# Kernel optimization log

Hardware: AMD Instinct MI355X
Metric: run time of the kernel (lower is better)

The kernel has to match this reference:

```python
import jax, jax.numpy as jnp
import numpy as np

MARGIN = 0.3
EPS = 0.1              # label smoothing weight
NUM_CLASSES = 100000
WEIGHT_T = 1.0
WEIGHT_X = 1.0
BATCH = 1024
EMBED_DIM = 512


def setup_inputs() -> dict:
    key = jax.random.key(0)
    k1, k2, k3 = jax.random.split(key, 3)
    x = jax.random.normal(k1, (BATCH, EMBED_DIM), dtype=jnp.float32)
    # classifier: weight ~ N(0, 0.01), bias = 0 (matches nn.init in module)
    W = jax.random.normal(k2, (NUM_CLASSES, EMBED_DIM), dtype=jnp.float32) * 0.01
    b = jnp.zeros((NUM_CLASSES,), dtype=jnp.float32)
    labels = jax.random.randint(k3, (BATCH,), 0, NUM_CLASSES)
    return {"x": x, "W": W, "b": b, "labels": labels}


def reference(x, W, b, labels):
    # ---- TripletLoss with batch-hard mining ----
    sq = jnp.sum(x * x, axis=1)                      # [B]
    dist = sq[:, None] + sq[None, :] - 2.0 * (x @ x.T)  # [B, B]
    dist = jnp.sqrt(jnp.clip(dist, 1e-12))
    same = labels[:, None] == labels[None, :]        # [B, B] (diagonal True)
    dist_ap = jnp.max(jnp.where(same, dist, -jnp.inf), axis=1)  # hardest positive
    dist_an = jnp.min(jnp.where(same, jnp.inf, dist), axis=1)   # hardest negative
    # MarginRankingLoss(dist_an, dist_ap, y=1) = mean(relu(dist_ap - dist_an + margin))
    triplet_loss = jnp.mean(jnp.maximum(dist_ap - dist_an + MARGIN, 0.0))

    # ---- CrossEntropy with label smoothing ----
    logits = x @ W.T + b                              # [B, K]
    log_probs = jax.nn.log_softmax(logits, axis=1)
    onehot = jax.nn.one_hot(labels, NUM_CLASSES, dtype=log_probs.dtype)
    targets = (1.0 - EPS) * onehot + EPS / NUM_CLASSES
    ce_loss = jnp.sum(jnp.mean(-targets * log_probs, axis=0))

    return WEIGHT_T * triplet_loss + WEIGHT_X * ce_loss
```

## Files before the change

### kernel.cpp

```cpp
#include <hip/hip_runtime.h>
#include <hip/hip_bf16.h>
#include <math.h>

#define B 1024
#define D 512
#define KC 100000
#define MARGIN 0.3f
#define EPSSM 0.1f
#define NCP 782
#define NCP_PAD 784

typedef __attribute__((ext_vector_type(8))) short bf16x8;
typedef __attribute__((ext_vector_type(4))) float f32x4;

__device__ __forceinline__ unsigned cvtpk(float lo, float hi) {
    union { __hip_bfloat162 h2; unsigned u; } cv;
    cv.h2 = __float22bfloat162_rn(make_float2(lo, hi));
    return cv.u;
}

__device__ __forceinline__ void async16(const void* g, void* l) {
    __builtin_amdgcn_global_load_lds((const __attribute__((address_space(1))) unsigned int*)g,
                                     (__attribute__((address_space(3))) unsigned int*)l,
                                     16, 0, 0);
}

#define VMCNT(n) asm volatile("s_waitcnt vmcnt(" #n ")" ::: "memory")
#define FENCE    asm volatile("" ::: "memory")


__global__ void init_ws(float* ws) {
    int i = blockIdx.x * blockDim.x + threadIdx.x;
    if (i < 2 * B) ws[i] = 0.f;
    else if (i < 3 * B) ((int*)ws)[i] = 0;
    else if (i < 4 * B) ((int*)ws)[i] = 0x7F800000;
}

__global__ __launch_bounds__(256) void prep_kernel(const float* __restrict__ x,
                                                   const float* __restrict__ W,
                                                   const float* __restrict__ bias,
                                                   const int* __restrict__ labels,
                                                   float* __restrict__ ws,
                                                   unsigned short* __restrict__ xp) {
    const int bid = blockIdx.x;
    const int tid = threadIdx.x;
    __shared__ float xs[8][D];
    __shared__ int labs[8];
    __shared__ float sqi[8];
    __shared__ float red_ap[8][4], red_an[8][4];

    if (bid >= 512) {
        int gid = (bid - 512) * 256 + tid;
        int region = gid >> 9;
        int u = gid & 511;
        int rloc = u >> 2, qpos = u & 3;
        int ku = qpos ^ ((rloc >> 1) & 3);
        int mb = region >> 4, kt = region & 15;
        const float* src = x + (size_t)(mb * 128 + rloc) * D + kt * 32 + ku * 8;
        f32x4 a = *(const f32x4*)src;
        f32x4 b2 = *(const f32x4*)(src + 4);
        unsigned pv[4] = { cvtpk(a[0], a[1]), cvtpk(a[2], a[3]), cvtpk(b2[0], b2[1]), cvtpk(b2[2], b2[3]) };
        *(uint4*)(xp + (size_t)region * 4096 + (size_t)u * 8) = *(uint4*)pv;
        return;
    }
    if (bid >= 256) {
        int wid = tid >> 6, lane = tid & 63;
        int row = (bid - 256) * 4 + wid;
        int lab = labels[row];
        const float* xr = x + (size_t)row * D;
        const float* wr = W + (size_t)lab * D;
        float dsum = 0.f;
#pragma unroll
        for (int u = 0; u < 2; ++u) {
            int k = (lane * 2 + u) * 4;
            float4 a = *(const float4*)&xr[k];
            float4 w = *(const float4*)&wr[k];
            dsum += a.x * w.x + a.y * w.y + a.z * w.z + a.w * w.w;
        }
        for (int o = 32; o >= 1; o >>= 1) dsum += __shfl_xor(dsum, o);
        if (lane == 0) atomicAdd(&ws[B + row], (1.f - EPSSM) * (dsum + bias[lab]));
        return;
    }

    const int row0 = (bid >> 1) * 8;
    const int jbase = (bid & 1) * 512;
    for (int f = tid; f < 8 * (D / 4); f += 256) {
        int r = f / (D / 4);
        int p = f % (D / 4);
        *(float4*)&xs[r][p * 4] = *(const float4*)&x[(size_t)(row0 + r) * D + p * 4];
    }
    if (tid < 8) labs[tid] = labels[row0 + tid];
    __syncthreads();
    if (tid < 8) {
        float s = 0.f;
        for (int k = 0; k < D; ++k) s += xs[tid][k] * xs[tid][k];
        sqi[tid] = s;
    }
    __syncthreads();

    float ap[8], an[8];
#pragma unroll
    for (int r = 0; r < 8; ++r) { ap[r] = -INFINITY; an[r] = INFINITY; }

    for (int j = jbase + tid; j < jbase + 512; j += 256) {
        int labj = labels[j];
        float dot[8];
        float sqj = 0.f;
#pragma unroll
        for (int r = 0; r < 8; ++r) dot[r] = 0.f;
        for (int kc = 0; kc < D; kc += 32) {
            float4 xj[8];
#pragma unroll
            for (int u = 0; u < 8; ++u) xj[u] = *(const float4*)&x[(size_t)j * D + kc + u * 4];
#pragma unroll
            for (int u = 0; u < 8; ++u)
                sqj += xj[u].x * xj[u].x + xj[u].y * xj[u].y + xj[u].z * xj[u].z + xj[u].w * xj[u].w;
#pragma unroll
            for (int r = 0; r < 8; ++r) {
                float d = 0.f;
#pragma unroll
                for (int u = 0; u < 8; ++u) {
                    const float4 a = *(const float4*)&xs[r][kc + u * 4];
                    d += a.x * xj[u].x + a.y * xj[u].y + a.z * xj[u].z + a.w * xj[u].w;
                }
                dot[r] += d;
            }
        }
#pragma unroll
        for (int r = 0; r < 8; ++r) {
            float d2 = sqi[r] + sqj - 2.f * dot[r];
            float dist = sqrtf(fmaxf(d2, 1e-12f));
            if (labj == labs[r]) ap[r] = fmaxf(ap[r], dist);
            else an[r] = fminf(an[r], dist);
        }
    }
#pragma unroll
    for (int r = 0; r < 8; ++r) {
        for (int o = 32; o >= 1; o >>= 1) {
            ap[r] = fmaxf(ap[r], __shfl_xor(ap[r], o));
            an[r] = fminf(an[r], __shfl_xor(an[r], o));
        }
    }
    int wid = tid >> 6;
    if ((tid & 63) == 0) {
#pragma unroll
        for (int r = 0; r < 8; ++r) { red_ap[r][wid] = ap[r]; red_an[r][wid] = an[r]; }
    }
    __syncthreads();
    if (tid < 8) {
        float a = -INFINITY, n = INFINITY;
#pragma unroll
        for (int w = 0; w < 4; ++w) { a = fmaxf(a, red_ap[tid][w]); n = fminf(n, red_an[tid][w]); }
        a = fmaxf(a, 0.f);
        int* apbits = (int*)(ws + 2 * B);
        int* anbits = (int*)(ws + 3 * B);
        atomicMax(&apbits[row0 + tid], __float_as_int(a));
        atomicMin(&anbits[row0 + tid], __float_as_int(n));
    }
}

__global__ __launch_bounds__(256, 3) void ce_gemm_d(const unsigned short* __restrict__ xp,
                                                    const float* __restrict__ W,
                                                    const float* __restrict__ bias,
                                                    float* __restrict__ ws) {
    const int b = blockIdx.x;
    const int xcd = b & 7, slot = b >> 3;
    const int cp = (slot >> 3) * 8 + xcd;
    const int mb = slot & 7;
    if (cp >= NCP) return;
    const int rowbase = mb * 128;
    const int cbase = cp * 128;

    __shared__ unsigned short lds[24576];

    const int tid = threadIdx.x;
    const int lane = tid & 63;
    const int wid = tid >> 6;
    const int wm = wid >> 1, wn = wid & 1;
    const int q = lane >> 4, l15 = lane & 15;

    f32x4 acc[4][4];
#pragma unroll
    for (int m = 0; m < 4; ++m)
#pragma unroll
        for (int n = 0; n < 4; ++n) acc[m][n] = (f32x4){0.f, 0.f, 0.f, 0.f};

#define STAGE(kt_) {                                                               \
        unsigned short* lA = &lds[((kt_) & 1) * 12288];                            \
        float* lB = (float*)&lds[((kt_) & 1) * 12288 + 4096];                      \
        const unsigned short* ga = xp + (size_t)(mb * 16 + (kt_)) * 4096;          \
        async16(ga + tid * 8, lA + tid * 8);                                       \
        async16(ga + 2048 + tid * 8, lA + 2048 + tid * 8);                         \
        _Pragma("unroll")                                                          \
        for (int i = 0; i < 4; ++i) {                                              \
            int u = i * 256 + tid;                                                 \
            int row = u >> 3;                                                      \
            int lu = (u & 7) ^ (row & 7);                                          \
            int rc = cbase + row; rc = rc < KC ? rc : KC - 1;                      \
            async16(&W[(size_t)rc * D + (kt_) * 32 + lu * 4], lB + u * 4);         \
        } }
#define READS(par_) {                                                              \
        const unsigned short* sA = &lds[(par_) * 12288];                           \
        const float* sB = (const float*)&lds[(par_) * 12288 + 4096];               \
        _Pragma("unroll") for (int m = 0; m < 4; ++m) {                            \
            int rl = wm * 64 + m * 16 + l15;                                       \
            af[m] = *(const bf16x8*)&sA[(rl * 4 + (q ^ ((rl >> 1) & 3))) * 8]; }   \
        _Pragma("unroll") for (int n = 0; n < 4; ++n) {                            \
            int rl = wn * 64 + n * 16 + l15;                                       \
            f32x4 b0 = *(const f32x4*)&sB[rl * 32 + ((q * 2) ^ (rl & 7)) * 4];     \
            f32x4 b1 = *(const f32x4*)&sB[rl * 32 + ((q * 2 + 1) ^ (rl & 7)) * 4]; \
            union { unsigned u[4]; bf16x8 v; } cv;                                 \
            cv.u[0] = cvtpk(b0[0], b0[1]); cv.u[1] = cvtpk(b0[2], b0[3]);          \
            cv.u[2] = cvtpk(b1[0], b1[1]); cv.u[3] = cvtpk(b1[2], b1[3]);          \
            bfr[n] = cv.v; } }
#define MFMAC() {                                                                  \
        __builtin_amdgcn_s_setprio(1);                                             \
        _Pragma("unroll") for (int m = 0; m < 4; ++m)                              \
        _Pragma("unroll") for (int n = 0; n < 4; ++n)                              \
            acc[m][n] = __builtin_amdgcn_mfma_f32_16x16x32_bf16(                   \
                af[m], bfr[n], acc[m][n], 0, 0, 0);                                \
        __builtin_amdgcn_s_setprio(0); }

    STAGE(0); STAGE(1);

    bf16x8 af[4], bfr[4];
#pragma unroll
    for (int kt = 0; kt < 16; ++kt) {
        const int par = kt & 1;
        if (kt < 15) { VMCNT(6); } else { VMCNT(0); }
        __builtin_amdgcn_s_barrier(); FENCE;
        READS(par);
        MFMAC();
        __builtin_amdgcn_s_barrier(); FENCE;
        if (kt + 2 < 16) STAGE(kt + 2);
    }
#undef STAGE
#undef READS
#undef MFMAC

    __syncthreads();
    float* redE = (float*)lds;
    float* redL = redE + 256;
    float biasv[4];
#pragma unroll
    for (int n = 0; n < 4; ++n) {
        int cc = cbase + wn * 64 + n * 16 + l15;
        biasv[n] = bias[cc < KC ? cc : KC - 1];
    }
#pragma unroll
    for (int m = 0; m < 4; ++m) {
#pragma unroll
        for (int r2 = 0; r2 < 4; ++r2) {
            float pe = 0.f, pl = 0.f;
#pragma unroll
            for (int n = 0; n < 4; ++n) {
                int cc = cbase + wn * 64 + n * 16 + l15;
                if (cc < KC) {
                    float lg = acc[m][n][r2] + biasv[n];
                    pe += __expf(lg);
                    pl += lg;
                }
            }
#pragma unroll
            for (int o = 1; o < 16; o <<= 1) {
                pe += __shfl_xor(pe, o);
                pl += __shfl_xor(pl, o);
            }
            if (l15 == 0) {
                int rowl = wm * 64 + m * 16 + q * 4 + r2;
                redE[rowl * 2 + wn] = pe;
                redL[rowl * 2 + wn] = pl;
            }
        }
    }
    __syncthreads();
    if (tid < 128) {
        float se = redE[tid * 2] + redE[tid * 2 + 1];
        float sl = redL[tid * 2] + redL[tid * 2 + 1];
        atomicAdd(&ws[rowbase + tid], se);
        atomicAdd(&ws[B + rowbase + tid], (EPSSM / (float)KC) * sl);
    }
}

__global__ __launch_bounds__(1024) void final_kernel(const float* __restrict__ ws,
                                                     float* __restrict__ out) {
    const float* sumexp = ws;
    const float* lin = ws + B;
    const int* apbits = (const int*)(ws + 2 * B);
    const int* anbits = (const int*)(ws + 3 * B);
    int i = threadIdx.x;
    float ce = logf(sumexp[i]) - lin[i];
    float ap = __int_as_float(apbits[i]);
    float an = __int_as_float(anbits[i]);
    float v = ce + fmaxf(ap - an + MARGIN, 0.f);
    for (int o = 32; o >= 1; o >>= 1) v += __shfl_xor(v, o);
    __shared__ float red[16];
    int wid = threadIdx.x >> 6, lane = threadIdx.x & 63;
    if (lane == 0) red[wid] = v;
    __syncthreads();
    if (threadIdx.x == 0) {
        float s = 0.f;
#pragma unroll
        for (int w = 0; w < 16; ++w) s += red[w];
        out[0] = s / (float)B;
    }
}

extern "C" void kernel_launch(void* const* d_in, const int* in_sizes, int n_in,
                              void* d_out, int out_size, void* d_ws, size_t ws_size,
                              hipStream_t stream) {
    const float* x = (const float*)d_in[0];
    const float* W = (const float*)d_in[1];
    const float* bias = (const float*)d_in[2];
    const int* labels = (const int*)d_in[3];
    float* out = (float*)d_out;
    float* ws = (float*)d_ws;

    unsigned short* xp = (unsigned short*)((char*)d_ws + 16384);

    init_ws<<<16, 256, 0, stream>>>(ws);
    prep_kernel<<<768, 256, 0, stream>>>(x, W, bias, labels, ws, xp);
    ce_gemm_d<<<8 * NCP_PAD, 256, 0, stream>>>(xp, W, bias, ws);
    final_kernel<<<1, 1024, 0, stream>>>(ws, out);
}
```

Measured before the change: 265.4 us.

## Enlarge CE GEMM tile to 256 rows, convert W to bf16 once in LDS

Raises the CE GEMM block tile from 128 to 256 batch rows, so each W tile is read from global memory half as many times, and launches half as many blocks. W is now loaded into registers three k-steps ahead, converted to bf16 by one thread, and written once into a double-buffered LDS slot. Previously every wave re-read fp32 W from LDS and converted it itself. The packed activations use a triple-buffered LDS ring with a matching 256-row packing layout in the prep kernel. The cost is 32 accumulator tiles per thread and more register pressure, with occupancy dropped to 2 blocks per SIMD group.

```diff
diff --git a/kernel.cpp b/kernel.cpp
--- a/kernel.cpp
+++ b/kernel.cpp
@@ -26,6 +26,7 @@
 }
 
 #define VMCNT(n) asm volatile("s_waitcnt vmcnt(" #n ")" ::: "memory")
+#define LGKM0    asm volatile("s_waitcnt lgkmcnt(0)" ::: "memory")
 #define FENCE    asm volatile("" ::: "memory")
 
 
@@ -51,16 +52,16 @@
 
     if (bid >= 512) {
         int gid = (bid - 512) * 256 + tid;
-        int region = gid >> 9;
-        int u = gid & 511;
-        int rloc = u >> 2, qpos = u & 3;
+        int region = gid >> 10;
+        int p = gid & 1023;
+        int rloc = p >> 2, qpos = p & 3;
         int ku = qpos ^ ((rloc >> 1) & 3);
         int mb = region >> 4, kt = region & 15;
-        const float* src = x + (size_t)(mb * 128 + rloc) * D + kt * 32 + ku * 8;
+        const float* src = x + (size_t)(mb * 256 + rloc) * D + kt * 32 + ku * 8;
         f32x4 a = *(const f32x4*)src;
         f32x4 b2 = *(const f32x4*)(src + 4);
         unsigned pv[4] = { cvtpk(a[0], a[1]), cvtpk(a[2], a[3]), cvtpk(b2[0], b2[1]), cvtpk(b2[2], b2[3]) };
-        *(uint4*)(xp + (size_t)region * 4096 + (size_t)u * 8) = *(uint4*)pv;
+        *(uint4*)(xp + (size_t)region * 8192 + (size_t)p * 8) = *(uint4*)pv;
         return;
     }
     if (bid >= 256) {
@@ -159,19 +160,19 @@
     }
 }
 
-__global__ __launch_bounds__(256, 3) void ce_gemm_d(const unsigned short* __restrict__ xp,
+__global__ __launch_bounds__(256, 2) void ce_gemm_r(const unsigned short* __restrict__ xp,
                                                     const float* __restrict__ W,
                                                     const float* __restrict__ bias,
                                                     float* __restrict__ ws) {
     const int b = blockIdx.x;
     const int xcd = b & 7, slot = b >> 3;
-    const int cp = (slot >> 3) * 8 + xcd;
-    const int mb = slot & 7;
+    const int cp = (slot >> 2) * 8 + xcd;
+    const int mb = slot & 3;
     if (cp >= NCP) return;
-    const int rowbase = mb * 128;
+    const int rowbase = mb * 256;
     const int cbase = cp * 128;
 
-    __shared__ unsigned short lds[24576];
+    __shared__ unsigned short lds[32768];
 
     const int tid = threadIdx.x;
     const int lane = tid & 63;
@@ -179,68 +180,93 @@
     const int wm = wid >> 1, wn = wid & 1;
     const int q = lane >> 4, l15 = lane & 15;
 
-    f32x4 acc[4][4];
-#pragma unroll
-    for (int m = 0; m < 4; ++m)
+    const int rB = tid >> 1;
+    const int ku0 = (tid & 1) * 2;
+    const int swB = (rB >> 1) & 3;
+    const int p0 = rB * 4 + (ku0 ^ swB);
+    const int p1 = rB * 4 + ((ku0 + 1) ^ swB);
+    int rc = cbase + rB; rc = rc < KC ? rc : KC - 1;
+    const float* pW = W + (size_t)rc * D + (tid & 1) * 16;
+
+    f32x4 acc[8][4];
+#pragma unroll
+    for (int m = 0; m < 8; ++m)
 #pragma unroll
         for (int n = 0; n < 4; ++n) acc[m][n] = (f32x4){0.f, 0.f, 0.f, 0.f};
 
-#define STAGE(kt_) {                                                               \
-        unsigned short* lA = &lds[((kt_) & 1) * 12288];                            \
-        float* lB = (float*)&lds[((kt_) & 1) * 12288 + 4096];                      \
-        const unsigned short* ga = xp + (size_t)(mb * 16 + (kt_)) * 4096;          \
-        async16(ga + tid * 8, lA + tid * 8);                                       \
-        async16(ga + 2048 + tid * 8, lA + 2048 + tid * 8);                         \
-        _Pragma("unroll")                                                          \
-        for (int i = 0; i < 4; ++i) {                                              \
-            int u = i * 256 + tid;                                                 \
-            int row = u >> 3;                                                      \
-            int lu = (u & 7) ^ (row & 7);                                          \
-            int rc = cbase + row; rc = rc < KC ? rc : KC - 1;                      \
-            async16(&W[(size_t)rc * D + (kt_) * 32 + lu * 4], lB + u * 4);         \
-        } }
-#define READS(par_) {                                                              \
-        const unsigned short* sA = &lds[(par_) * 12288];                           \
-        const float* sB = (const float*)&lds[(par_) * 12288 + 4096];               \
-        _Pragma("unroll") for (int m = 0; m < 4; ++m) {                            \
-            int rl = wm * 64 + m * 16 + l15;                                       \
-            af[m] = *(const bf16x8*)&sA[(rl * 4 + (q ^ ((rl >> 1) & 3))) * 8]; }   \
-        _Pragma("unroll") for (int n = 0; n < 4; ++n) {                            \
-            int rl = wn * 64 + n * 16 + l15;                                       \
-            f32x4 b0 = *(const f32x4*)&sB[rl * 32 + ((q * 2) ^ (rl & 7)) * 4];     \
-            f32x4 b1 = *(const f32x4*)&sB[rl * 32 + ((q * 2 + 1) ^ (rl & 7)) * 4]; \
-            union { unsigned u[4]; bf16x8 v; } cv;                                 \
-            cv.u[0] = cvtpk(b0[0], b0[1]); cv.u[1] = cvtpk(b0[2], b0[3]);          \
-            cv.u[2] = cvtpk(b1[0], b1[1]); cv.u[3] = cvtpk(b1[2], b1[3]);          \
-            bfr[n] = cv.v; } }
-#define MFMAC() {                                                                  \
-        __builtin_amdgcn_s_setprio(1);                                             \
-        _Pragma("unroll") for (int m = 0; m < 4; ++m)                              \
-        _Pragma("unroll") for (int n = 0; n < 4; ++n)                              \
-            acc[m][n] = __builtin_amdgcn_mfma_f32_16x16x32_bf16(                   \
-                af[m], bfr[n], acc[m][n], 0, 0, 0);                                \
-        __builtin_amdgcn_s_setprio(0); }
-
-    STAGE(0); STAGE(1);
+    f32x4 bsv[3][4];
+
+#define BLOAD(s_, kt_) {                                                           \
+        _Pragma("unroll") for (int j = 0; j < 4; ++j)                              \
+            bsv[s_][j] = *(const f32x4*)(pW + (kt_) * 32 + j * 4);                 \
+        FENCE; }
+#define ALOAD(kt_) {                                                               \
+        const unsigned short* ga = xp + (size_t)(mb * 16 + (kt_)) * 8192;          \
+        unsigned short* lA = &lds[((kt_) % 3) * 8192];                             \
+        _Pragma("unroll") for (int i = 0; i < 4; ++i)                              \
+            async16(ga + (i * 256 + tid) * 8, lA + (i * 256 + tid) * 8);           \
+        FENCE; }
+#define BCVW(s_, kt_) {                                                            \
+        unsigned short* lB = &lds[24576 + ((kt_) & 1) * 4096];                     \
+        unsigned u0[4] = { cvtpk(bsv[s_][0][0], bsv[s_][0][1]),                    \
+                           cvtpk(bsv[s_][0][2], bsv[s_][0][3]),                    \
+                           cvtpk(bsv[s_][1][0], bsv[s_][1][1]),                    \
+                           cvtpk(bsv[s_][1][2], bsv[s_][1][3]) };                  \
+        unsigned u1[4] = { cvtpk(bsv[s_][2][0], bsv[s_][2][1]),                    \
+                           cvtpk(bsv[s_][2][2], bsv[s_][2][3]),                    \
+                           cvtpk(bsv[s_][3][0], bsv[s_][3][1]),                    \
+                           cvtpk(bsv[s_][3][2], bsv[s_][3][3]) };                  \
+        *(uint4*)&lB[p0 * 8] = *(uint4*)u0;                                        \
+        *(uint4*)&lB[p1 * 8] = *(uint4*)u1; }
+
+    BLOAD(0, 0); BLOAD(1, 1); ALOAD(0); BLOAD(2, 2); ALOAD(1);
+    VMCNT(16);
+    BCVW(0, 0);
+    LGKM0;
 
     bf16x8 af[4], bfr[4];
 #pragma unroll
     for (int kt = 0; kt < 16; ++kt) {
-        const int par = kt & 1;
-        if (kt < 15) { VMCNT(6); } else { VMCNT(0); }
+        if (kt <= 13) { VMCNT(8); } else if (kt == 14) { VMCNT(4); } else { VMCNT(0); }
         __builtin_amdgcn_s_barrier(); FENCE;
-        READS(par);
-        MFMAC();
+
+        const unsigned short* sA = &lds[(kt % 3) * 8192];
+        const unsigned short* sB = &lds[24576 + (kt & 1) * 4096];
+#pragma unroll
+        for (int n = 0; n < 4; ++n) {
+            int rl = wn * 64 + n * 16 + l15;
+            bfr[n] = *(const bf16x8*)&sB[(rl * 4 + (q ^ ((rl >> 1) & 3))) * 8];
+        }
+#pragma unroll
+        for (int mg = 0; mg < 2; ++mg) {
+#pragma unroll
+            for (int mf = 0; mf < 4; ++mf) {
+                int rl = wm * 128 + (mg * 4 + mf) * 16 + l15;
+                af[mf] = *(const bf16x8*)&sA[(rl * 4 + (q ^ ((rl >> 1) & 3))) * 8];
+            }
+            __builtin_amdgcn_s_setprio(1);
+#pragma unroll
+            for (int mf = 0; mf < 4; ++mf)
+#pragma unroll
+                for (int n = 0; n < 4; ++n)
+                    acc[mg * 4 + mf][n] = __builtin_amdgcn_mfma_f32_16x16x32_bf16(
+                        af[mf], bfr[n], acc[mg * 4 + mf][n], 0, 0, 0);
+            __builtin_amdgcn_s_setprio(0);
+        }
+
+        if (kt < 15) BCVW((kt + 1) % 3, kt + 1);
+        if (kt <= 12) BLOAD((kt + 3) % 3, kt + 3);
+        if (kt <= 13) ALOAD(kt + 2);
+        LGKM0;
         __builtin_amdgcn_s_barrier(); FENCE;
-        if (kt + 2 < 16) STAGE(kt + 2);
-    }
-#undef STAGE
-#undef READS
-#undef MFMAC
+    }
+#undef BLOAD
+#undef ALOAD
+#undef BCVW
 
     __syncthreads();
     float* redE = (float*)lds;
-    float* redL = redE + 256;
+    float* redL = redE + 512;
     float biasv[4];
 #pragma unroll
     for (int n = 0; n < 4; ++n) {
@@ -248,7 +274,7 @@
         biasv[n] = bias[cc < KC ? cc : KC - 1];
     }
 #pragma unroll
-    for (int m = 0; m < 4; ++m) {
+    for (int m = 0; m < 8; ++m) {
 #pragma unroll
         for (int r2 = 0; r2 < 4; ++r2) {
             float pe = 0.f, pl = 0.f;
@@ -267,14 +293,14 @@
                 pl += __shfl_xor(pl, o);
             }
             if (l15 == 0) {
-                int rowl = wm * 64 + m * 16 + q * 4 + r2;
+                int rowl = wm * 128 + m * 16 + q * 4 + r2;
                 redE[rowl * 2 + wn] = pe;
                 redL[rowl * 2 + wn] = pl;
             }
         }
     }
     __syncthreads();
-    if (tid < 128) {
+    if (tid < 256) {
         float se = redE[tid * 2] + redE[tid * 2 + 1];
         float sl = redL[tid * 2] + redL[tid * 2 + 1];
         atomicAdd(&ws[rowbase + tid], se);
@@ -320,6 +346,6 @@
 
     init_ws<<<16, 256, 0, stream>>>(ws);
     prep_kernel<<<768, 256, 0, stream>>>(x, W, bias, labels, ws, xp);
-    ce_gemm_d<<<8 * NCP_PAD, 256, 0, stream>>>(xp, W, bias, ws);
+    ce_gemm_r<<<8 * (NCP_PAD / 8) * 4, 256, 0, stream>>>(xp, W, bias, ws);
     final_kernel<<<1, 1024, 0, stream>>>(ws, out);
 }
```

Result: faster. 219.3 us (median of 2 runs) (-17.4%).
